# Kernel optimization log

Hardware: AMD Instinct MI355X
Metric: run time of the kernel (lower is better)

## Reference

```python
import jax, jax.numpy as jnp
import numpy as np

B = 16384   # batch
S = 6       # fixed number of ABR frequencies
H = 8       # num_heads
HD = 64     # head_dim
D = H * HD  # model width = head_dim * num_heads


def _pe(d):
    # FrequencyPositionalEncoding: pe[i, 0::2] = sin(f_i * div), pe[i, 1::2] = cos(f_i * div)
    freqs = np.array([6.0, 12.0, 18.0, 24.0, 30.0, 0.0], np.float32) / 30.0
    div = np.exp(np.arange(0, d, 2, dtype=np.float32) * (-np.log(10000.0) / d))
    pe = np.zeros((S, d), np.float32)
    pe[:, 0::2] = np.sin(freqs[:, None] * div)
    pe[:, 1::2] = np.cos(freqs[:, None] * div)
    return jnp.asarray(pe)


def _freq_bias():
    # adjacent-frequency bias 0.1, octave pairs (0,1),(1,3) overwritten to 0.05
    b = np.zeros((S, S), np.float32)
    for i in range(S - 1):
        b[i, i + 1] = 0.1
        b[i + 1, i] = 0.1
    for i, j in [(0, 1), (1, 3)]:
        b[i, j] = 0.05
        b[j, i] = 0.05
    return jnp.asarray(b)


def setup_inputs() -> dict:
    key = jax.random.key(0)
    ks = jax.random.split(key, 6)

    def w(k, shape, s=0.05):
        return jax.random.normal(k, shape, jnp.float32) * s

    return {
        "x": jax.random.normal(ks[0], (B, S), jnp.float32),
        "W_in": w(ks[1], (1, D)), "b_in": jnp.zeros((D,), jnp.float32),
        "Wq": w(ks[2], (D, D)), "bq": jnp.zeros((D,), jnp.float32),
        "Wk": w(ks[3], (D, D)), "bk": jnp.zeros((D,), jnp.float32),
        "Wv": w(ks[4], (D, D)), "bv": jnp.zeros((D,), jnp.float32),
        "Wo": w(ks[5], (D, 1)), "bo": jnp.zeros((1,), jnp.float32),
        "gamma": jnp.ones((D,), jnp.float32),
        "beta": jnp.zeros((D,), jnp.float32),
    }


def reference(x, W_in, b_in, Wq, bq, Wk, bk, Wv, bv, Wo, bo, gamma, beta):
    Bn, Sn = x.shape
    Dn = gamma.shape[0]
    hd = Dn // H
    # input projection: scalar token -> D   (Linear(1, D))
    tok = x[..., None] * W_in[0] + b_in                      # (B, S, D)
    tok = tok + _pe(Dn)[None]                                # frequency positional encoding
    # LayerNorm (eps=1e-5)
    mu = tok.mean(-1, keepdims=True)
    var = tok.var(-1, keepdims=True)
    tok = (tok - mu) * jax.lax.rsqrt(var + 1e-5) * gamma + beta
    # q/k/v projections, split heads
    q = (tok @ Wq + bq).reshape(Bn, Sn, H, hd)
    k = (tok @ Wk + bk).reshape(Bn, Sn, H, hd)
    v = (tok @ Wv + bv).reshape(Bn, Sn, H, hd)
    scores = jnp.einsum('bihd,bjhd->bhij', q, k) * (hd ** -0.5)
    scores = scores + _freq_bias()[None, None]               # (B, H, S, S)
    attn = jax.nn.softmax(scores, axis=-1)                   # dropout = identity (eval)
    attended = jnp.einsum('bhij,bjhd->bihd', attn, v).reshape(Bn, Sn, Dn)
    out = (attended @ Wo + bo)[..., 0] + x                   # (B, S) residual
    return out, attn.mean(axis=1)
```

## Files before the change

kernel.cpp:

```cpp
#include <hip/hip_runtime.h>
#include <math.h>

#define WS_STATS 0
#define WS_T     16

__constant__ float FREQ_BIAS[36] = {
    0.0f, 0.05f, 0.0f, 0.0f, 0.0f, 0.0f,
    0.05f, 0.0f, 0.1f, 0.05f, 0.0f, 0.0f,
    0.0f, 0.1f, 0.0f, 0.1f, 0.0f, 0.0f,
    0.0f, 0.05f, 0.1f, 0.0f, 0.1f, 0.0f,
    0.0f, 0.0f, 0.0f, 0.1f, 0.0f, 0.1f,
    0.0f, 0.0f, 0.0f, 0.0f, 0.1f, 0.0f
};

__global__ __launch_bounds__(256) void kA(
    const float* __restrict__ W_in, const float* __restrict__ b_in,
    const float* __restrict__ gamma, const float* __restrict__ beta,
    const float* __restrict__ Wq, const float* __restrict__ bq,
    const float* __restrict__ Wk, const float* __restrict__ bk,
    const float* __restrict__ Wv, const float* __restrict__ bv,
    float* __restrict__ ws, float* __restrict__ part)
{
    __shared__ float ls[8][512];
    __shared__ float partial[4][8][64];
    __shared__ float red[13][4];

    const int tid = threadIdx.x, wave = tid >> 6, lane = tid & 63;
    const int bid = blockIdx.x;
    const int rc = bid & 7, cg = (bid >> 3) & 7, p = bid >> 6;

    const float k_ln = 0.0179889457300305367f;
    const float freqs[6] = {0.2f, 0.4f, 0.6f, 0.8f, 1.0f, 0.0f};
    float wd[2], cc2[2][6], gm[2], bt[2];
    #pragma unroll
    for (int q = 0; q < 2; ++q) {
        const int d = tid + q * 256;
        wd[q] = W_in[d];
        gm[q] = gamma[d];
        bt[q] = beta[d];
        float dv = __expf(-(float)(d & ~1) * k_ln);
        float bi = b_in[d];
        bool odd = (d & 1);
        #pragma unroll
        for (int s = 0; s < 6; ++s) {
            float ph = freqs[s] * dv;
            cc2[q][s] = bi + (odd ? __cosf(ph) : __sinf(ph));
        }
    }
    {
        float sums[7];
        sums[0] = wd[0] + wd[1];
        #pragma unroll
        for (int s = 0; s < 6; ++s) sums[1 + s] = cc2[0][s] + cc2[1][s];
        #pragma unroll
        for (int m = 1; m < 64; m <<= 1) {
            #pragma unroll
            for (int k = 0; k < 7; ++k) sums[k] += __shfl_xor(sums[k], m, 64);
        }
        if (lane == 0) {
            #pragma unroll
            for (int k = 0; k < 7; ++k) red[k][wave] = sums[k];
        }
    }
    __syncthreads();
    const float mw = (red[0][0] + red[0][1] + red[0][2] + red[0][3]) * (1.0f / 512.0f);
    float mc[6];
    #pragma unroll
    for (int s = 0; s < 6; ++s)
        mc[s] = (red[1 + s][0] + red[1 + s][1] + red[1 + s][2] + red[1 + s][3]) * (1.0f / 512.0f);
    __syncthreads();

    float hw[2], hc[2][6];
    #pragma unroll
    for (int q = 0; q < 2; ++q) {
        hw[q] = wd[q] - mw;
        #pragma unroll
        for (int s = 0; s < 6; ++s) hc[q][s] = cc2[q][s] - mc[s];
    }

    if (bid == 0) {
        float moms[13];
        moms[0] = hw[0] * hw[0] + hw[1] * hw[1];
        #pragma unroll
        for (int s = 0; s < 6; ++s) {
            moms[1 + s] = hw[0] * hc[0][s] + hw[1] * hc[1][s];
            moms[7 + s] = hc[0][s] * hc[0][s] + hc[1][s] * hc[1][s];
        }
        #pragma unroll
        for (int m = 1; m < 64; m <<= 1) {
            #pragma unroll
            for (int k = 0; k < 13; ++k) moms[k] += __shfl_xor(moms[k], m, 64);
        }
        if (lane == 0) {
            #pragma unroll
            for (int k = 0; k < 13; ++k) red[k][wave] = moms[k];
        }
    }
    #pragma unroll
    for (int q = 0; q < 2; ++q) {
        const int d = tid + q * 256;
        ls[0][d] = hw[q] * gm[q];
        #pragma unroll
        for (int s = 0; s < 6; ++s) ls[1 + s][d] = hc[q][s] * gm[q];
        ls[7][d] = bt[q];
    }
    __syncthreads();
    if (bid == 0 && tid < 13)
        ws[WS_STATS + tid] = (red[tid][0] + red[tid][1] + red[tid][2] + red[tid][3]) * (1.0f / 512.0f);

    const float* W  = (p == 0) ? Wq : ((p == 1) ? Wk : Wv);
    const float* bb = (p == 0) ? bq : ((p == 1) ? bk : bv);
    const int col = (cg << 6) | lane;
    const int row0 = (rc << 6) | (wave << 4);
    float acc[8] = {0.f, 0.f, 0.f, 0.f, 0.f, 0.f, 0.f, 0.f};
    #pragma unroll
    for (int rr = 0; rr < 16; ++rr) {
        const float wv = W[(row0 + rr) * 512 + col];
        #pragma unroll
        for (int v = 0; v < 8; ++v) acc[v] = fmaf(wv, ls[v][row0 + rr], acc[v]);
    }
    #pragma unroll
    for (int v = 0; v < 8; ++v) partial[wave][v][lane] = acc[v];
    __syncthreads();
    #pragma unroll
    for (int ii = 0; ii < 2; ++ii) {
        const int idx = tid + ii * 256;
        const int v = idx >> 6, cx = idx & 63;
        float t = partial[0][v][cx] + partial[1][v][cx]
                + partial[2][v][cx] + partial[3][v][cx];
        if (v == 7 && rc == 0) t += bb[(cg << 6) | cx];
        part[(size_t)bid * 512 + idx] = t;
    }
}

__global__ __launch_bounds__(256) void kB(const float* __restrict__ part,
                                          const float* __restrict__ Wo,
                                          float* __restrict__ ws)
{
    __shared__ float ab[24][65];
    const int tid = threadIdx.x;
    const int h = blockIdx.x;

    for (int e = tid; e < 24 * 64; e += 256) {
        const int vp = e >> 6, c = e & 63;
        const int p = vp >> 3, v = vp & 7;
        const int stripe = p * 8 + h;
        float t = 0.f;
        #pragma unroll
        for (int rcx = 0; rcx < 8; ++rcx)
            t += part[(size_t)(stripe * 8 + rcx) * 512 + v * 64 + c];
        ab[vp][c] = t;
    }
    __syncthreads();

    if (tid < 64) {
        const int a = tid >> 3, b2 = tid & 7;
        float acc = 0.f;
        #pragma unroll
        for (int c = 0; c < 64; ++c)
            acc = fmaf(ab[a][c], ab[8 + b2][c], acc);
        ws[WS_T + (h << 6) + tid] = acc * 0.125f;
    } else if (tid < 72) {
        const int a = tid - 64;
        float acc = 0.f;
        #pragma unroll
        for (int c = 0; c < 64; ++c)
            acc = fmaf(ab[16 + a][c], Wo[(h << 6) + c], acc);
        ws[WS_T + 512 + (h << 3) + a] = acc;
    }
}

__global__ __launch_bounds__(256) void kC(const float* __restrict__ x,
                                          const float* __restrict__ ws,
                                          const float* __restrict__ bo,
                                          float* __restrict__ out, int total)
{
    __shared__ float T_s[592];
    const int tid = threadIdx.x;
    for (int e = tid; e < 589; e += 256)
        T_s[e] = (e < 576) ? ws[WS_T + e] : ws[WS_STATS + (e - 576)];
    __syncthreads();

    const int g = blockIdx.x * 256 + tid;
    if (g >= total) return;
    const unsigned b = (unsigned)g / 6u;
    const int i = g - (int)b * 6;

    const float* D8 = T_s;
    const float* VD = T_s + 512;
    const float vw = T_s[576];
    const float* cov = T_s + 577;
    const float* vc = T_s + 583;
    const float bo0 = bo[0];

    const float2* xp = (const float2*)(x + (size_t)b * 6u);
    const float2 x01 = xp[0], x23 = xp[1], x45 = xp[2];
    const float al[6] = {x01.x, x01.y, x23.x, x23.y, x45.x, x45.y};

    float r[6], u[6];
    #pragma unroll
    for (int j = 0; j < 6; ++j) {
        float a = al[j];
        float var = fmaf(a, fmaf(a, vw, 2.0f * cov[j]), vc[j]) + 1e-5f;
        r[j] = rsqrtf(var);
        u[j] = a * r[j];
    }

    float bias[6];
    #pragma unroll
    for (int j = 0; j < 6; ++j) bias[j] = FREQ_BIAS[i * 6 + j];

    const float r_i = r[i], u_i = u[i];
    float acc = 0.f;
    float am[6] = {0.f, 0.f, 0.f, 0.f, 0.f, 0.f};

    #pragma unroll
    for (int h = 0; h < 8; ++h) {
        const float* Dh = D8 + h * 64;
        const float* Vh = VD + h * 8;
        const float P1 = Dh[0], P5 = Dh[7], P7 = Dh[56], P9 = Dh[63];
        const float P3i = Dh[(1 + i) * 8], P6i = Dh[(1 + i) * 8 + 7];

        float s[6];
        #pragma unroll
        for (int j = 0; j < 6; ++j) {
            float t1 = fmaf(u[j], P1, fmaf(r[j], Dh[1 + j], P5));
            float t2 = fmaf(u[j], P3i, fmaf(r[j], Dh[(1 + i) * 8 + 1 + j], P6i));
            float t3 = fmaf(u[j], P7, fmaf(r[j], Dh[57 + j], P9));
            s[j] = fmaf(u_i, t1, fmaf(r_i, t2, t3)) + bias[j];
        }
        float m = s[0];
        #pragma unroll
        for (int j = 1; j < 6; ++j) m = fmaxf(m, s[j]);
        float e[6], ssum = 0.f;
        #pragma unroll
        for (int j = 0; j < 6; ++j) { e[j] = __expf(s[j] - m); ssum += e[j]; }
        const float inv = 1.0f / ssum;

        const float av = Vh[0], cvv = Vh[7];
        float ha = 0.f;
        #pragma unroll
        for (int j = 0; j < 6; ++j) {
            float a = e[j] * inv;
            am[j] += a;
            float vp = fmaf(u[j], av, r[j] * Vh[1 + j]);
            ha = fmaf(a, vp, ha);
        }
        acc += ha + cvv;
    }

    out[g] = acc + bo0 + al[i];

    float2* amp = (float2*)(out + total + (size_t)g * 6u);
    amp[0] = make_float2(am[0] * 0.125f, am[1] * 0.125f);
    amp[1] = make_float2(am[2] * 0.125f, am[3] * 0.125f);
    amp[2] = make_float2(am[4] * 0.125f, am[5] * 0.125f);
}

extern "C" void kernel_launch(void* const* d_in, const int* in_sizes, int n_in,
                              void* d_out, int out_size, void* d_ws, size_t ws_size,
                              hipStream_t stream) {
    const float* x     = (const float*)d_in[0];
    const float* W_in  = (const float*)d_in[1];
    const float* b_in  = (const float*)d_in[2];
    const float* Wq    = (const float*)d_in[3];
    const float* bq    = (const float*)d_in[4];
    const float* Wk    = (const float*)d_in[5];
    const float* bk    = (const float*)d_in[6];
    const float* Wv    = (const float*)d_in[7];
    const float* bv    = (const float*)d_in[8];
    const float* Wo    = (const float*)d_in[9];
    const float* bo    = (const float*)d_in[10];
    const float* gamma = (const float*)d_in[11];
    const float* beta  = (const float*)d_in[12];
    float* ws  = (float*)d_ws;
    float* out = (float*)d_out;

    const int total = in_sizes[0];

    kA<<<192, 256, 0, stream>>>(W_in, b_in, gamma, beta, Wq, bq, Wk, bk, Wv, bv, ws, out);
    kB<<<8, 256, 0, stream>>>(out, Wo, ws);
    kC<<<(total + 255) / 256, 256, 0, stream>>>(x, ws, bo, out, total);
}
```

Before: 20.63 us.

## Merge three-kernel pipeline into two by fusing head reductions into consumer

The projection kernel now uses 24 blocks of 1024 threads. Each block covers all 512 rows for one column group, reducing across waves in shared memory instead of writing row-chunk partials to global memory. The separate per-head reduction kernel is removed, and every block of the final kernel recomputes the small 8x8 per-head score tables and Wo dot products from the projected vectors. This saves a launch and a global round trip, but gives up parallelism in the projection stage (24 blocks instead of 192) and repeats the small reduction work in each consumer block.

```diff
diff --git a/kernel.cpp b/kernel.cpp
--- a/kernel.cpp
+++ b/kernel.cpp
@@ -2,7 +2,7 @@
 #include <math.h>
 
 #define WS_STATS 0
-#define WS_T     16
+#define WS_AB    16
 
 __constant__ float FREQ_BIAS[36] = {
     0.0f, 0.05f, 0.0f, 0.0f, 0.0f, 0.0f,
@@ -13,172 +13,191 @@
     0.0f, 0.0f, 0.0f, 0.0f, 0.1f, 0.0f
 };
 
-__global__ __launch_bounds__(256) void kA(
+__global__ __launch_bounds__(1024) void kA2(
     const float* __restrict__ W_in, const float* __restrict__ b_in,
     const float* __restrict__ gamma, const float* __restrict__ beta,
     const float* __restrict__ Wq, const float* __restrict__ bq,
     const float* __restrict__ Wk, const float* __restrict__ bk,
     const float* __restrict__ Wv, const float* __restrict__ bv,
-    float* __restrict__ ws, float* __restrict__ part)
+    float* __restrict__ ws)
 {
-    __shared__ float ls[8][512];
-    __shared__ float partial[4][8][64];
-    __shared__ float red[13][4];
-
-    const int tid = threadIdx.x, wave = tid >> 6, lane = tid & 63;
+    __shared__ float ls_f[512 * 9];
+    __shared__ float buf[8 * 512];
+    __shared__ float red[13][8];
+
+    const int tid = threadIdx.x, lane = tid & 63, wave = tid >> 6;
     const int bid = blockIdx.x;
-    const int rc = bid & 7, cg = (bid >> 3) & 7, p = bid >> 6;
-
-    const float k_ln = 0.0179889457300305367f;
-    const float freqs[6] = {0.2f, 0.4f, 0.6f, 0.8f, 1.0f, 0.0f};
-    float wd[2], cc2[2][6], gm[2], bt[2];
-    #pragma unroll
-    for (int q = 0; q < 2; ++q) {
-        const int d = tid + q * 256;
-        wd[q] = W_in[d];
-        gm[q] = gamma[d];
-        bt[q] = beta[d];
-        float dv = __expf(-(float)(d & ~1) * k_ln);
-        float bi = b_in[d];
-        bool odd = (d & 1);
+    const int p = bid >> 3, cg = bid & 7;
+
+    float wd = 0.f, gm = 0.f, bt = 0.f;
+    float c[6] = {0.f, 0.f, 0.f, 0.f, 0.f, 0.f};
+    if (tid < 512) {
+        const int d = tid;
+        const float k_ln = 0.0179889457300305367f;
+        const float freqs[6] = {0.2f, 0.4f, 0.6f, 0.8f, 1.0f, 0.0f};
+        wd = W_in[d]; gm = gamma[d]; bt = beta[d];
+        const float bi = b_in[d];
+        const float dv = __expf(-(float)(d & ~1) * k_ln);
+        const bool odd = (d & 1);
         #pragma unroll
         for (int s = 0; s < 6; ++s) {
             float ph = freqs[s] * dv;
-            cc2[q][s] = bi + (odd ? __cosf(ph) : __sinf(ph));
-        }
-    }
+            c[s] = bi + (odd ? __cosf(ph) : __sinf(ph));
+        }
+        float sums[7];
+        sums[0] = wd;
+        #pragma unroll
+        for (int s = 0; s < 6; ++s) sums[1 + s] = c[s];
+        #pragma unroll
+        for (int m = 1; m < 64; m <<= 1) {
+            #pragma unroll
+            for (int k = 0; k < 7; ++k) sums[k] += __shfl_xor(sums[k], m, 64);
+        }
+        if (lane == 0) {
+            #pragma unroll
+            for (int k = 0; k < 7; ++k) red[k][wave] = sums[k];
+        }
+    }
+    __syncthreads();
+    float mw = 0.f, mc[6];
     {
-        float sums[7];
-        sums[0] = wd[0] + wd[1];
-        #pragma unroll
-        for (int s = 0; s < 6; ++s) sums[1 + s] = cc2[0][s] + cc2[1][s];
+        float t = 0.f;
+        #pragma unroll
+        for (int j = 0; j < 8; ++j) t += red[0][j];
+        mw = t * (1.0f / 512.0f);
+        #pragma unroll
+        for (int s = 0; s < 6; ++s) {
+            t = 0.f;
+            #pragma unroll
+            for (int j = 0; j < 8; ++j) t += red[1 + s][j];
+            mc[s] = t * (1.0f / 512.0f);
+        }
+    }
+    __syncthreads();
+    if (tid < 512) {
+        const int d = tid;
+        const float hw = wd - mw;
+        float hc[6];
+        #pragma unroll
+        for (int s = 0; s < 6; ++s) hc[s] = c[s] - mc[s];
+        float moms[13];
+        moms[0] = hw * hw;
+        #pragma unroll
+        for (int s = 0; s < 6; ++s) { moms[1 + s] = hw * hc[s]; moms[7 + s] = hc[s] * hc[s]; }
         #pragma unroll
         for (int m = 1; m < 64; m <<= 1) {
             #pragma unroll
-            for (int k = 0; k < 7; ++k) sums[k] += __shfl_xor(sums[k], m, 64);
+            for (int k = 0; k < 13; ++k) moms[k] += __shfl_xor(moms[k], m, 64);
         }
         if (lane == 0) {
             #pragma unroll
-            for (int k = 0; k < 7; ++k) red[k][wave] = sums[k];
-        }
+            for (int k = 0; k < 13; ++k) red[k][wave] = moms[k];
+        }
+        ls_f[d * 9 + 0] = hw * gm;
+        #pragma unroll
+        for (int s = 0; s < 6; ++s) ls_f[d * 9 + 1 + s] = hc[s] * gm;
+        ls_f[d * 9 + 7] = bt;
     }
     __syncthreads();
-    const float mw = (red[0][0] + red[0][1] + red[0][2] + red[0][3]) * (1.0f / 512.0f);
-    float mc[6];
-    #pragma unroll
-    for (int s = 0; s < 6; ++s)
-        mc[s] = (red[1 + s][0] + red[1 + s][1] + red[1 + s][2] + red[1 + s][3]) * (1.0f / 512.0f);
-    __syncthreads();
-
-    float hw[2], hc[2][6];
-    #pragma unroll
-    for (int q = 0; q < 2; ++q) {
-        hw[q] = wd[q] - mw;
-        #pragma unroll
-        for (int s = 0; s < 6; ++s) hc[q][s] = cc2[q][s] - mc[s];
-    }
-
-    if (bid == 0) {
-        float moms[13];
-        moms[0] = hw[0] * hw[0] + hw[1] * hw[1];
-        #pragma unroll
-        for (int s = 0; s < 6; ++s) {
-            moms[1 + s] = hw[0] * hc[0][s] + hw[1] * hc[1][s];
-            moms[7 + s] = hc[0][s] * hc[0][s] + hc[1][s] * hc[1][s];
-        }
-        #pragma unroll
-        for (int m = 1; m < 64; m <<= 1) {
-            #pragma unroll
-            for (int k = 0; k < 13; ++k) moms[k] += __shfl_xor(moms[k], m, 64);
-        }
-        if (lane == 0) {
-            #pragma unroll
-            for (int k = 0; k < 13; ++k) red[k][wave] = moms[k];
-        }
-    }
-    #pragma unroll
-    for (int q = 0; q < 2; ++q) {
-        const int d = tid + q * 256;
-        ls[0][d] = hw[q] * gm[q];
-        #pragma unroll
-        for (int s = 0; s < 6; ++s) ls[1 + s][d] = hc[q][s] * gm[q];
-        ls[7][d] = bt[q];
-    }
-    __syncthreads();
-    if (bid == 0 && tid < 13)
-        ws[WS_STATS + tid] = (red[tid][0] + red[tid][1] + red[tid][2] + red[tid][3]) * (1.0f / 512.0f);
-
-    const float* W  = (p == 0) ? Wq : ((p == 1) ? Wk : Wv);
-    const float* bb = (p == 0) ? bq : ((p == 1) ? bk : bv);
+    if (bid == 0 && tid < 13) {
+        float t = 0.f;
+        #pragma unroll
+        for (int j = 0; j < 8; ++j) t += red[tid][j];
+        ws[WS_STATS + tid] = t * (1.0f / 512.0f);
+    }
+
+    const int rb = wave * 32;
+    const int r0 = rb + (lane >> 3), v0 = lane & 7;
+    const float h0 = ls_f[(r0)      * 9 + v0];
+    const float h1 = ls_f[(r0 + 8)  * 9 + v0];
+    const float h2 = ls_f[(r0 + 16) * 9 + v0];
+    const float h3 = ls_f[(r0 + 24) * 9 + v0];
+
+    const float* W = (p == 0) ? Wq : ((p == 1) ? Wk : Wv);
     const int col = (cg << 6) | lane;
-    const int row0 = (rc << 6) | (wave << 4);
     float acc[8] = {0.f, 0.f, 0.f, 0.f, 0.f, 0.f, 0.f, 0.f};
     #pragma unroll
-    for (int rr = 0; rr < 16; ++rr) {
-        const float wv = W[(row0 + rr) * 512 + col];
-        #pragma unroll
-        for (int v = 0; v < 8; ++v) acc[v] = fmaf(wv, ls[v][row0 + rr], acc[v]);
-    }
-    #pragma unroll
-    for (int v = 0; v < 8; ++v) partial[wave][v][lane] = acc[v];
-    __syncthreads();
-    #pragma unroll
-    for (int ii = 0; ii < 2; ++ii) {
-        const int idx = tid + ii * 256;
-        const int v = idx >> 6, cx = idx & 63;
-        float t = partial[0][v][cx] + partial[1][v][cx]
-                + partial[2][v][cx] + partial[3][v][cx];
-        if (v == 7 && rc == 0) t += bb[(cg << 6) | cx];
-        part[(size_t)bid * 512 + idx] = t;
+    for (int rr = 0; rr < 32; ++rr) {
+        const float wv = W[(rb + rr) * 512 + col];
+        const float hreg = (rr < 8) ? h0 : (rr < 16) ? h1 : (rr < 24) ? h2 : h3;
+        #pragma unroll
+        for (int v = 0; v < 8; ++v) {
+            const float s = __int_as_float(
+                __builtin_amdgcn_readlane(__float_as_int(hreg), (rr & 7) * 8 + v));
+            acc[v] = fmaf(wv, s, acc[v]);
+        }
+    }
+
+    #pragma unroll
+    for (int n = 16; n > 1; n >>= 1) {
+        const int half = n >> 1;
+        if (wave >= half && wave < n) {
+            #pragma unroll
+            for (int v = 0; v < 8; ++v)
+                buf[(wave - half) * 512 + v * 64 + lane] = acc[v];
+        }
+        __syncthreads();
+        if (wave < half) {
+            #pragma unroll
+            for (int v = 0; v < 8; ++v)
+                acc[v] += buf[wave * 512 + v * 64 + lane];
+        }
+        __syncthreads();
+    }
+    if (wave == 0) {
+        const float* bb = (p == 0) ? bq : ((p == 1) ? bk : bv);
+        #pragma unroll
+        for (int v = 0; v < 8; ++v) {
+            float t = acc[v];
+            if (v == 7) t += bb[col];
+            ws[WS_AB + ((p * 8 + v) << 9) + col] = t;
+        }
     }
 }
 
-__global__ __launch_bounds__(256) void kB(const float* __restrict__ part,
-                                          const float* __restrict__ Wo,
-                                          float* __restrict__ ws)
-{
-    __shared__ float ab[24][65];
-    const int tid = threadIdx.x;
-    const int h = blockIdx.x;
-
-    for (int e = tid; e < 24 * 64; e += 256) {
-        const int vp = e >> 6, c = e & 63;
-        const int p = vp >> 3, v = vp & 7;
-        const int stripe = p * 8 + h;
-        float t = 0.f;
-        #pragma unroll
-        for (int rcx = 0; rcx < 8; ++rcx)
-            t += part[(size_t)(stripe * 8 + rcx) * 512 + v * 64 + c];
-        ab[vp][c] = t;
-    }
-    __syncthreads();
-
-    if (tid < 64) {
-        const int a = tid >> 3, b2 = tid & 7;
-        float acc = 0.f;
-        #pragma unroll
-        for (int c = 0; c < 64; ++c)
-            acc = fmaf(ab[a][c], ab[8 + b2][c], acc);
-        ws[WS_T + (h << 6) + tid] = acc * 0.125f;
-    } else if (tid < 72) {
-        const int a = tid - 64;
-        float acc = 0.f;
-        #pragma unroll
-        for (int c = 0; c < 64; ++c)
-            acc = fmaf(ab[16 + a][c], Wo[(h << 6) + c], acc);
-        ws[WS_T + 512 + (h << 3) + a] = acc;
-    }
-}
-
-__global__ __launch_bounds__(256) void kC(const float* __restrict__ x,
-                                          const float* __restrict__ ws,
-                                          const float* __restrict__ bo,
-                                          float* __restrict__ out, int total)
+__global__ __launch_bounds__(256) void kC2(const float* __restrict__ x,
+                                           const float* __restrict__ ws,
+                                           const float* __restrict__ Wo,
+                                           const float* __restrict__ bo,
+                                           float* __restrict__ out, int total)
 {
     __shared__ float T_s[592];
     const int tid = threadIdx.x;
-    for (int e = tid; e < 589; e += 256)
-        T_s[e] = (e < 576) ? ws[WS_T + e] : ws[WS_STATS + (e - 576)];
+
+    #pragma unroll
+    for (int ee = 0; ee < 2; ++ee) {
+        const int e = tid + ee * 256;
+        const int h = e >> 6, a = (e >> 3) & 7, b2 = e & 7;
+        const float4* qv = (const float4*)(ws + WS_AB + a * 512 + h * 64);
+        const float4* kv = (const float4*)(ws + WS_AB + (8 + b2) * 512 + h * 64);
+        float acc = 0.f;
+        #pragma unroll
+        for (int cc = 0; cc < 16; ++cc) {
+            float4 q = qv[cc], k = kv[cc];
+            acc = fmaf(q.x, k.x, acc);
+            acc = fmaf(q.y, k.y, acc);
+            acc = fmaf(q.z, k.z, acc);
+            acc = fmaf(q.w, k.w, acc);
+        }
+        T_s[e] = acc * 0.125f;
+    }
+    if (tid < 64) {
+        const int h = tid >> 3, a = tid & 7;
+        const float4* vv = (const float4*)(ws + WS_AB + (16 + a) * 512 + h * 64);
+        const float4* wo = (const float4*)(Wo + h * 64);
+        float acc = 0.f;
+        #pragma unroll
+        for (int cc = 0; cc < 16; ++cc) {
+            float4 v = vv[cc], w = wo[cc];
+            acc = fmaf(v.x, w.x, acc);
+            acc = fmaf(v.y, w.y, acc);
+            acc = fmaf(v.z, w.z, acc);
+            acc = fmaf(v.w, w.w, acc);
+        }
+        T_s[512 + tid] = acc;
+    } else if (tid < 77) {
+        T_s[576 + tid - 64] = ws[WS_STATS + tid - 64];
+    }
     __syncthreads();
 
     const int g = blockIdx.x * 256 + tid;
@@ -278,7 +297,6 @@
 
     const int total = in_sizes[0];
 
-    kA<<<192, 256, 0, stream>>>(W_in, b_in, gamma, beta, Wq, bq, Wk, bk, Wv, bv, ws, out);
-    kB<<<8, 256, 0, stream>>>(out, Wo, ws);
-    kC<<<(total + 255) / 256, 256, 0, stream>>>(x, ws, bo, out, total);
+    kA2<<<24, 1024, 0, stream>>>(W_in, b_in, gamma, beta, Wq, bq, Wk, bk, Wv, bv, ws);
+    kC2<<<(total + 255) / 256, 256, 0, stream>>>(x, ws, Wo, bo, out, total);
 }
```

New measurement: 29.76 us. 1.44x slower.

## Fuse reduction kernel into per-block recompute, cutting launches from three to two

Applied to the files above, without the earlier changes.

Replaces the three-kernel pipeline with two kernels when enough workspace is available. The projection kernel now uses 96 blocks with 4 row-chunk partials written to workspace, and the final kernel has each 1024-thread block redundantly reduce those partials and compute the small head-interaction tables before running the per-element attention. This removes one kernel launch and its serialization, at the cost of every block repeating the table computation and reading about 192KB of partials. The shared LN-folded activations are also transposed to a row-major [512][8] layout so they can be read as float4.

```diff
diff --git a/kernel.cpp b/kernel.cpp
--- a/kernel.cpp
+++ b/kernel.cpp
@@ -3,6 +3,8 @@
 
 #define WS_STATS 0
 #define WS_T     16
+#define WS_P     1024
+#define WS_NEED  ((WS_P + 4 * 24 * 512) * sizeof(float))
 
 __constant__ float FREQ_BIAS[36] = {
     0.0f, 0.05f, 0.0f, 0.0f, 0.0f, 0.0f,
@@ -13,22 +15,12 @@
     0.0f, 0.0f, 0.0f, 0.0f, 0.1f, 0.0f
 };
 
-__global__ __launch_bounds__(256) void kA(
+__device__ __forceinline__ void ln_fold_phase(
     const float* __restrict__ W_in, const float* __restrict__ b_in,
     const float* __restrict__ gamma, const float* __restrict__ beta,
-    const float* __restrict__ Wq, const float* __restrict__ bq,
-    const float* __restrict__ Wk, const float* __restrict__ bk,
-    const float* __restrict__ Wv, const float* __restrict__ bv,
-    float* __restrict__ ws, float* __restrict__ part)
-{
-    __shared__ float ls[8][512];
-    __shared__ float partial[4][8][64];
-    __shared__ float red[13][4];
-
-    const int tid = threadIdx.x, wave = tid >> 6, lane = tid & 63;
-    const int bid = blockIdx.x;
-    const int rc = bid & 7, cg = (bid >> 3) & 7, p = bid >> 6;
-
+    float* __restrict__ ws, float (*ls8)[8], float (*red)[4],
+    int tid, int wave, int lane, bool do_stats)
+{
     const float k_ln = 0.0179889457300305367f;
     const float freqs[6] = {0.2f, 0.4f, 0.6f, 0.8f, 1.0f, 0.0f};
     float wd[2], cc2[2][6], gm[2], bt[2];
@@ -77,8 +69,7 @@
         #pragma unroll
         for (int s = 0; s < 6; ++s) hc[q][s] = cc2[q][s] - mc[s];
     }
-
-    if (bid == 0) {
+    if (do_stats) {
         float moms[13];
         moms[0] = hw[0] * hw[0] + hw[1] * hw[1];
         #pragma unroll
@@ -99,14 +90,203 @@
     #pragma unroll
     for (int q = 0; q < 2; ++q) {
         const int d = tid + q * 256;
-        ls[0][d] = hw[q] * gm[q];
-        #pragma unroll
-        for (int s = 0; s < 6; ++s) ls[1 + s][d] = hc[q][s] * gm[q];
-        ls[7][d] = bt[q];
-    }
-    __syncthreads();
-    if (bid == 0 && tid < 13)
+        ls8[d][0] = hw[q] * gm[q];
+        #pragma unroll
+        for (int s = 0; s < 6; ++s) ls8[d][1 + s] = hc[q][s] * gm[q];
+        ls8[d][7] = bt[q];
+    }
+    __syncthreads();
+    if (do_stats && tid < 13)
         ws[WS_STATS + tid] = (red[tid][0] + red[tid][1] + red[tid][2] + red[tid][3]) * (1.0f / 512.0f);
+}
+
+
+__global__ __launch_bounds__(256) void kA3(
+    const float* __restrict__ W_in, const float* __restrict__ b_in,
+    const float* __restrict__ gamma, const float* __restrict__ beta,
+    const float* __restrict__ Wq, const float* __restrict__ bq,
+    const float* __restrict__ Wk, const float* __restrict__ bk,
+    const float* __restrict__ Wv, const float* __restrict__ bv,
+    float* __restrict__ ws)
+{
+    __shared__ float ls8[512][8];
+    __shared__ float partial[4][8][64];
+    __shared__ float red[13][4];
+
+    const int tid = threadIdx.x, wave = tid >> 6, lane = tid & 63;
+    const int bid = blockIdx.x;
+    const int rc = bid & 3, cg = (bid >> 2) & 7, p = bid >> 5;
+
+    ln_fold_phase(W_in, b_in, gamma, beta, ws, ls8, red, tid, wave, lane, bid == 0);
+
+    const float* W  = (p == 0) ? Wq : ((p == 1) ? Wk : Wv);
+    const float* bb = (p == 0) ? bq : ((p == 1) ? bk : bv);
+    const int col = (cg << 6) | lane;
+    const int row0 = (rc << 7) | (wave << 5);
+
+    float acc[8] = {0.f, 0.f, 0.f, 0.f, 0.f, 0.f, 0.f, 0.f};
+    #pragma unroll
+    for (int rr = 0; rr < 32; ++rr) {
+        const int row = row0 + rr;
+        const float wv = W[row * 512 + col];
+        const float4 f0 = *(const float4*)&ls8[row][0];
+        const float4 f1 = *(const float4*)&ls8[row][4];
+        acc[0] = fmaf(wv, f0.x, acc[0]);
+        acc[1] = fmaf(wv, f0.y, acc[1]);
+        acc[2] = fmaf(wv, f0.z, acc[2]);
+        acc[3] = fmaf(wv, f0.w, acc[3]);
+        acc[4] = fmaf(wv, f1.x, acc[4]);
+        acc[5] = fmaf(wv, f1.y, acc[5]);
+        acc[6] = fmaf(wv, f1.z, acc[6]);
+        acc[7] = fmaf(wv, f1.w, acc[7]);
+    }
+    #pragma unroll
+    for (int v = 0; v < 8; ++v) partial[wave][v][lane] = acc[v];
+    __syncthreads();
+    #pragma unroll
+    for (int ii = 0; ii < 2; ++ii) {
+        const int idx = tid + ii * 256;
+        const int v = idx >> 6, cx = idx & 63;
+        float t = partial[0][v][cx] + partial[1][v][cx]
+                + partial[2][v][cx] + partial[3][v][cx];
+        if (v == 7 && rc == 0) t += bb[(cg << 6) | cx];
+        ws[WS_P + rc * 12288 + ((p * 8 + v) << 9) + ((cg << 6) | cx)] = t;
+    }
+}
+
+__global__ __launch_bounds__(1024) void kC3(const float* __restrict__ x,
+                                            const float* __restrict__ ws,
+                                            const float* __restrict__ Wo,
+                                            const float* __restrict__ bo,
+                                            float* __restrict__ out, int total)
+{
+    __shared__ float ab[24][516];
+    __shared__ float T_s[592];
+    __shared__ float xs[1040];
+    const int tid = threadIdx.x;
+    const int g0 = blockIdx.x * 1024;
+
+    for (int e = tid; e < 12288; e += 1024) {
+        const int vp = e >> 9, col = e & 511;
+        float t = ws[WS_P + e] + ws[WS_P + 12288 + e]
+                + ws[WS_P + 24576 + e] + ws[WS_P + 36864 + e];
+        ab[vp][col] = t;
+    }
+    const int base = (g0 / 6) * 6;
+    const int cnt = min(1040, total - base);
+    for (int idx = tid; idx < cnt; idx += 1024) xs[idx] = x[base + idx];
+    if (tid < 13) T_s[576 + tid] = ws[WS_STATS + tid];
+    __syncthreads();
+
+    if (tid < 512) {
+        const int h = tid >> 6, a = (tid >> 3) & 7, b2 = tid & 7;
+        float acc = 0.f;
+        #pragma unroll
+        for (int c = 0; c < 64; ++c)
+            acc = fmaf(ab[a][(h << 6) + c], ab[8 + b2][(h << 6) + c], acc);
+        T_s[tid] = acc * 0.125f;
+    } else if (tid < 576) {
+        const int u = tid - 512, h = u >> 3, a = u & 7;
+        float acc = 0.f;
+        #pragma unroll
+        for (int c = 0; c < 64; ++c)
+            acc = fmaf(ab[16 + a][(h << 6) + c], Wo[(h << 6) + c], acc);
+        T_s[tid] = acc;
+    }
+    __syncthreads();
+
+    const int g = g0 + tid;
+    if (g >= total) return;
+    const unsigned b = (unsigned)g / 6u;
+    const int i = g - (int)b * 6;
+
+    const float* D8 = T_s;
+    const float* VD = T_s + 512;
+    const float vw = T_s[576];
+    const float* cov = T_s + 577;
+    const float* vc = T_s + 583;
+    const float bo0 = bo[0];
+
+    const int xoff = g - base - i;
+    float al[6], r[6], u[6];
+    #pragma unroll
+    for (int j = 0; j < 6; ++j) {
+        float a = xs[xoff + j];
+        al[j] = a;
+        float var = fmaf(a, fmaf(a, vw, 2.0f * cov[j]), vc[j]) + 1e-5f;
+        r[j] = rsqrtf(var);
+        u[j] = a * r[j];
+    }
+
+    float bias[6];
+    #pragma unroll
+    for (int j = 0; j < 6; ++j) bias[j] = FREQ_BIAS[i * 6 + j];
+
+    const float r_i = r[i], u_i = u[i];
+    float acc = 0.f;
+    float am[6] = {0.f, 0.f, 0.f, 0.f, 0.f, 0.f};
+
+    #pragma unroll
+    for (int h = 0; h < 8; ++h) {
+        const float* Dh = D8 + h * 64;
+        const float* Vh = VD + h * 8;
+        const float P1 = Dh[0], P5 = Dh[7], P7 = Dh[56], P9 = Dh[63];
+        const float P3i = Dh[(1 + i) * 8], P6i = Dh[(1 + i) * 8 + 7];
+
+        float s[6];
+        #pragma unroll
+        for (int j = 0; j < 6; ++j) {
+            float t1 = fmaf(u[j], P1, fmaf(r[j], Dh[1 + j], P5));
+            float t2 = fmaf(u[j], P3i, fmaf(r[j], Dh[(1 + i) * 8 + 1 + j], P6i));
+            float t3 = fmaf(u[j], P7, fmaf(r[j], Dh[57 + j], P9));
+            s[j] = fmaf(u_i, t1, fmaf(r_i, t2, t3)) + bias[j];
+        }
+        float m = s[0];
+        #pragma unroll
+        for (int j = 1; j < 6; ++j) m = fmaxf(m, s[j]);
+        float e[6], ssum = 0.f;
+        #pragma unroll
+        for (int j = 0; j < 6; ++j) { e[j] = __expf(s[j] - m); ssum += e[j]; }
+        const float inv = 1.0f / ssum;
+
+        const float av = Vh[0], cvv = Vh[7];
+        float ha = 0.f;
+        #pragma unroll
+        for (int j = 0; j < 6; ++j) {
+            float a = e[j] * inv;
+            am[j] += a;
+            float vp = fmaf(u[j], av, r[j] * Vh[1 + j]);
+            ha = fmaf(a, vp, ha);
+        }
+        acc += ha + cvv;
+    }
+
+    out[g] = acc + bo0 + al[i];
+
+    float2* amp = (float2*)(out + total + (size_t)g * 6u);
+    amp[0] = make_float2(am[0] * 0.125f, am[1] * 0.125f);
+    amp[1] = make_float2(am[2] * 0.125f, am[3] * 0.125f);
+    amp[2] = make_float2(am[4] * 0.125f, am[5] * 0.125f);
+}
+
+
+__global__ __launch_bounds__(256) void kA(
+    const float* __restrict__ W_in, const float* __restrict__ b_in,
+    const float* __restrict__ gamma, const float* __restrict__ beta,
+    const float* __restrict__ Wq, const float* __restrict__ bq,
+    const float* __restrict__ Wk, const float* __restrict__ bk,
+    const float* __restrict__ Wv, const float* __restrict__ bv,
+    float* __restrict__ ws, float* __restrict__ part)
+{
+    __shared__ float ls8[512][8];
+    __shared__ float partial[4][8][64];
+    __shared__ float red[13][4];
+
+    const int tid = threadIdx.x, wave = tid >> 6, lane = tid & 63;
+    const int bid = blockIdx.x;
+    const int rc = bid & 7, cg = (bid >> 3) & 7, p = bid >> 6;
+
+    ln_fold_phase(W_in, b_in, gamma, beta, ws, ls8, red, tid, wave, lane, bid == 0);
 
     const float* W  = (p == 0) ? Wq : ((p == 1) ? Wk : Wv);
     const float* bb = (p == 0) ? bq : ((p == 1) ? bk : bv);
@@ -115,9 +295,18 @@
     float acc[8] = {0.f, 0.f, 0.f, 0.f, 0.f, 0.f, 0.f, 0.f};
     #pragma unroll
     for (int rr = 0; rr < 16; ++rr) {
-        const float wv = W[(row0 + rr) * 512 + col];
-        #pragma unroll
-        for (int v = 0; v < 8; ++v) acc[v] = fmaf(wv, ls[v][row0 + rr], acc[v]);
+        const int row = row0 + rr;
+        const float wv = W[row * 512 + col];
+        const float4 f0 = *(const float4*)&ls8[row][0];
+        const float4 f1 = *(const float4*)&ls8[row][4];
+        acc[0] = fmaf(wv, f0.x, acc[0]);
+        acc[1] = fmaf(wv, f0.y, acc[1]);
+        acc[2] = fmaf(wv, f0.z, acc[2]);
+        acc[3] = fmaf(wv, f0.w, acc[3]);
+        acc[4] = fmaf(wv, f1.x, acc[4]);
+        acc[5] = fmaf(wv, f1.y, acc[5]);
+        acc[6] = fmaf(wv, f1.z, acc[6]);
+        acc[7] = fmaf(wv, f1.w, acc[7]);
     }
     #pragma unroll
     for (int v = 0; v < 8; ++v) partial[wave][v][lane] = acc[v];
@@ -205,7 +394,6 @@
         r[j] = rsqrtf(var);
         u[j] = a * r[j];
     }
-
     float bias[6];
     #pragma unroll
     for (int j = 0; j < 6; ++j) bias[j] = FREQ_BIAS[i * 6 + j];
@@ -250,7 +438,6 @@
     }
 
     out[g] = acc + bo0 + al[i];
-
     float2* amp = (float2*)(out + total + (size_t)g * 6u);
     amp[0] = make_float2(am[0] * 0.125f, am[1] * 0.125f);
     amp[1] = make_float2(am[2] * 0.125f, am[3] * 0.125f);
@@ -278,7 +465,12 @@
 
     const int total = in_sizes[0];
 
-    kA<<<192, 256, 0, stream>>>(W_in, b_in, gamma, beta, Wq, bq, Wk, bk, Wv, bv, ws, out);
-    kB<<<8, 256, 0, stream>>>(out, Wo, ws);
-    kC<<<(total + 255) / 256, 256, 0, stream>>>(x, ws, bo, out, total);
-}
+    if (ws_size >= WS_NEED) {
+        kA3<<<96, 256, 0, stream>>>(W_in, b_in, gamma, beta, Wq, bq, Wk, bk, Wv, bv, ws);
+        kC3<<<(total + 1023) / 1024, 1024, 0, stream>>>(x, ws, Wo, bo, out, total);
+    } else {
+        kA<<<192, 256, 0, stream>>>(W_in, b_in, gamma, beta, Wq, bq, Wk, bk, Wv, bv, ws, out);
+        kB<<<8, 256, 0, stream>>>(out, Wo, ws);
+        kC<<<(total + 255) / 256, 256, 0, stream>>>(x, ws, bo, out, total);
+    }
+}
```

Measured after the change: 27.30 us. 32.3% more time.

## Fuse reduction stage into projection kernel via last-block atomic counter

Applied to the files above, without the earlier changes.

Replaces the separate kB launch with a last-block-done pattern inside the projection kernel. Each block publishes its partials and bumps an atomic counter, and the final block does the cross-stripe reduction and the per-head products. This removes one kernel launch and its dependency gap, but adds a memset launch and leaves a single block doing the serial tail work. It also changes the LayerNorm-fold shared buffer to a row-major [512][8] layout so the GEMV inner loop can read it with float4 loads.

```diff
diff --git a/kernel.cpp b/kernel.cpp
--- a/kernel.cpp
+++ b/kernel.cpp
@@ -3,6 +3,9 @@
 
 #define WS_STATS 0
 #define WS_T     16
+#define WS_CNT   600
+#define WS_P     1024
+#define WS_NEED  ((WS_P + 192 * 512) * sizeof(float))
 
 __constant__ float FREQ_BIAS[36] = {
     0.0f, 0.05f, 0.0f, 0.0f, 0.0f, 0.0f,
@@ -13,22 +16,17 @@
     0.0f, 0.0f, 0.0f, 0.0f, 0.1f, 0.0f
 };
 
-__global__ __launch_bounds__(256) void kA(
+union KAU {
+    struct { float ls8[512][8]; float partial[4][8][64]; } a;
+    float ab[24][516];
+};
+
+__device__ __forceinline__ void ln_fold_phase(
     const float* __restrict__ W_in, const float* __restrict__ b_in,
     const float* __restrict__ gamma, const float* __restrict__ beta,
-    const float* __restrict__ Wq, const float* __restrict__ bq,
-    const float* __restrict__ Wk, const float* __restrict__ bk,
-    const float* __restrict__ Wv, const float* __restrict__ bv,
-    float* __restrict__ ws, float* __restrict__ part)
+    float* __restrict__ ws, float (*ls8)[8], float (*red)[4],
+    int tid, int wave, int lane, bool do_stats)
 {
-    __shared__ float ls[8][512];
-    __shared__ float partial[4][8][64];
-    __shared__ float red[13][4];
-
-    const int tid = threadIdx.x, wave = tid >> 6, lane = tid & 63;
-    const int bid = blockIdx.x;
-    const int rc = bid & 7, cg = (bid >> 3) & 7, p = bid >> 6;
-
     const float k_ln = 0.0179889457300305367f;
     const float freqs[6] = {0.2f, 0.4f, 0.6f, 0.8f, 1.0f, 0.0f};
     float wd[2], cc2[2][6], gm[2], bt[2];
@@ -77,8 +75,7 @@
         #pragma unroll
         for (int s = 0; s < 6; ++s) hc[q][s] = cc2[q][s] - mc[s];
     }
-
-    if (bid == 0) {
+    if (do_stats) {
         float moms[13];
         moms[0] = hw[0] * hw[0] + hw[1] * hw[1];
         #pragma unroll
@@ -99,14 +96,35 @@
     #pragma unroll
     for (int q = 0; q < 2; ++q) {
         const int d = tid + q * 256;
-        ls[0][d] = hw[q] * gm[q];
-        #pragma unroll
-        for (int s = 0; s < 6; ++s) ls[1 + s][d] = hc[q][s] * gm[q];
-        ls[7][d] = bt[q];
-    }
-    __syncthreads();
-    if (bid == 0 && tid < 13)
+        ls8[d][0] = hw[q] * gm[q];
+        #pragma unroll
+        for (int s = 0; s < 6; ++s) ls8[d][1 + s] = hc[q][s] * gm[q];
+        ls8[d][7] = bt[q];
+    }
+    __syncthreads();
+    if (do_stats && tid < 13)
         ws[WS_STATS + tid] = (red[tid][0] + red[tid][1] + red[tid][2] + red[tid][3]) * (1.0f / 512.0f);
+}
+
+template<bool TAIL>
+__global__ __launch_bounds__(256) void kAx(
+    const float* __restrict__ W_in, const float* __restrict__ b_in,
+    const float* __restrict__ gamma, const float* __restrict__ beta,
+    const float* __restrict__ Wq, const float* __restrict__ bq,
+    const float* __restrict__ Wk, const float* __restrict__ bk,
+    const float* __restrict__ Wv, const float* __restrict__ bv,
+    const float* __restrict__ Wo,
+    float* __restrict__ ws, float* __restrict__ part)
+{
+    __shared__ KAU U;
+    __shared__ float red[13][4];
+    __shared__ int win;
+
+    const int tid = threadIdx.x, wave = tid >> 6, lane = tid & 63;
+    const int bid = blockIdx.x;
+    const int rc = bid & 7, cg = (bid >> 3) & 7, p = bid >> 6;
+
+    ln_fold_phase(W_in, b_in, gamma, beta, ws, U.a.ls8, red, tid, wave, lane, bid == 0);
 
     const float* W  = (p == 0) ? Wq : ((p == 1) ? Wk : Wv);
     const float* bb = (p == 0) ? bq : ((p == 1) ? bk : bv);
@@ -115,21 +133,78 @@
     float acc[8] = {0.f, 0.f, 0.f, 0.f, 0.f, 0.f, 0.f, 0.f};
     #pragma unroll
     for (int rr = 0; rr < 16; ++rr) {
-        const float wv = W[(row0 + rr) * 512 + col];
-        #pragma unroll
-        for (int v = 0; v < 8; ++v) acc[v] = fmaf(wv, ls[v][row0 + rr], acc[v]);
-    }
-    #pragma unroll
-    for (int v = 0; v < 8; ++v) partial[wave][v][lane] = acc[v];
+        const int row = row0 + rr;
+        const float wv = W[row * 512 + col];
+        const float4 f0 = *(const float4*)&U.a.ls8[row][0];
+        const float4 f1 = *(const float4*)&U.a.ls8[row][4];
+        acc[0] = fmaf(wv, f0.x, acc[0]);
+        acc[1] = fmaf(wv, f0.y, acc[1]);
+        acc[2] = fmaf(wv, f0.z, acc[2]);
+        acc[3] = fmaf(wv, f0.w, acc[3]);
+        acc[4] = fmaf(wv, f1.x, acc[4]);
+        acc[5] = fmaf(wv, f1.y, acc[5]);
+        acc[6] = fmaf(wv, f1.z, acc[6]);
+        acc[7] = fmaf(wv, f1.w, acc[7]);
+    }
+    #pragma unroll
+    for (int v = 0; v < 8; ++v) U.a.partial[wave][v][lane] = acc[v];
     __syncthreads();
     #pragma unroll
     for (int ii = 0; ii < 2; ++ii) {
         const int idx = tid + ii * 256;
         const int v = idx >> 6, cx = idx & 63;
-        float t = partial[0][v][cx] + partial[1][v][cx]
-                + partial[2][v][cx] + partial[3][v][cx];
+        float t = U.a.partial[0][v][cx] + U.a.partial[1][v][cx]
+                + U.a.partial[2][v][cx] + U.a.partial[3][v][cx];
         if (v == 7 && rc == 0) t += bb[(cg << 6) | cx];
-        part[(size_t)bid * 512 + idx] = t;
+        if (TAIL) {
+            __hip_atomic_store(&part[(size_t)bid * 512 + idx], t,
+                               __ATOMIC_RELAXED, __HIP_MEMORY_SCOPE_AGENT);
+        } else {
+            part[(size_t)bid * 512 + idx] = t;
+        }
+    }
+
+    if (!TAIL) return;
+
+    asm volatile("s_waitcnt vmcnt(0)" ::: "memory");
+    __syncthreads();
+    if (tid == 0) {
+        int old = __hip_atomic_fetch_add((int*)ws + WS_CNT, 1,
+                                         __ATOMIC_ACQ_REL, __HIP_MEMORY_SCOPE_AGENT);
+        win = (old == 191);
+    }
+    __syncthreads();
+    if (!win) return;
+
+    for (int e4 = tid; e4 < 3072; e4 += 256) {
+        const int vp = e4 >> 7, c4 = e4 & 127;
+        const int pp = vp >> 3, v = vp & 7, cgg = c4 >> 4, cx4 = (c4 & 15) << 2;
+        float4 s = make_float4(0.f, 0.f, 0.f, 0.f);
+        #pragma unroll
+        for (int r = 0; r < 8; ++r) {
+            const float4 t4 = *(const float4*)&part[(size_t)(((pp << 6) | (cgg << 3) | r)) * 512 + (v << 6) + cx4];
+            s.x += t4.x; s.y += t4.y; s.z += t4.z; s.w += t4.w;
+        }
+        *(float4*)&U.ab[vp][c4 << 2] = s;
+    }
+    __syncthreads();
+    #pragma unroll
+    for (int ee = 0; ee < 2; ++ee) {
+        const int e = tid + ee * 256;
+        const int h = e >> 6, a2 = (e >> 3) & 7, b2 = e & 7;
+        float acc2 = 0.f;
+        #pragma unroll
+        for (int c = 0; c < 64; ++c)
+            acc2 = fmaf(U.ab[a2][(h << 6) + c], U.ab[8 + b2][(h << 6) + c], acc2);
+        ws[WS_T + e] = acc2 * 0.125f;
+    }
+    if (tid < 64) {
+        const int h = tid >> 3, a2 = tid & 7;
+        float acc2 = 0.f;
+        #pragma unroll
+        for (int c = 0; c < 64; ++c)
+            acc2 = fmaf(U.ab[16 + a2][(h << 6) + c], Wo[(h << 6) + c], acc2);
+        ws[WS_T + 512 + tid] = acc2;
     }
 }
 
@@ -205,7 +280,6 @@
         r[j] = rsqrtf(var);
         u[j] = a * r[j];
     }
-
     float bias[6];
     #pragma unroll
     for (int j = 0; j < 6; ++j) bias[j] = FREQ_BIAS[i * 6 + j];
@@ -250,7 +324,6 @@
     }
 
     out[g] = acc + bo0 + al[i];
-
     float2* amp = (float2*)(out + total + (size_t)g * 6u);
     amp[0] = make_float2(am[0] * 0.125f, am[1] * 0.125f);
     amp[1] = make_float2(am[2] * 0.125f, am[3] * 0.125f);
@@ -278,7 +351,15 @@
 
     const int total = in_sizes[0];
 
-    kA<<<192, 256, 0, stream>>>(W_in, b_in, gamma, beta, Wq, bq, Wk, bk, Wv, bv, ws, out);
-    kB<<<8, 256, 0, stream>>>(out, Wo, ws);
-    kC<<<(total + 255) / 256, 256, 0, stream>>>(x, ws, bo, out, total);
-}
+    if (ws_size >= WS_NEED) {
+        hipMemsetAsync((char*)d_ws + WS_CNT * sizeof(float), 0, sizeof(int), stream);
+        kAx<true><<<192, 256, 0, stream>>>(W_in, b_in, gamma, beta, Wq, bq, Wk, bk,
+                                           Wv, bv, Wo, ws, ws + WS_P);
+        kC<<<(total + 255) / 256, 256, 0, stream>>>(x, ws, bo, out, total);
+    } else {
+        kAx<false><<<192, 256, 0, stream>>>(W_in, b_in, gamma, beta, Wq, bq, Wk, bk,
+                                            Wv, bv, Wo, ws, out);
+        kB<<<8, 256, 0, stream>>>(out, Wo, ws);
+        kC<<<(total + 255) / 256, 256, 0, stream>>>(x, ws, bo, out, total);
+    }
+}
```

After: 31.38 us. 52.1% more time.
